# Performance work log

Measured on AMD Instinct MI355X. Metric: run time of the kernel, lower is better.

The kernel has to match this reference:

```python
import jax, jax.numpy as jnp
import numpy as np
from jax import lax

B, T, I, H, L, C = 256, 512, 128, 256, 2, 10


def _lstm_layer(x_tm, lengths, W_ih, W_hh, b_ih, b_hh):
    # x_tm: [T, B, in]; lengths: [B]
    b = b_ih + b_hh  # [4H]
    h0 = jnp.zeros((x_tm.shape[1], H), x_tm.dtype)
    c0 = jnp.zeros_like(h0)

    def step(carry, inp):
        h, c = carry
        x_t, t = inp
        gates = x_t @ W_ih.T + h @ W_hh.T + b  # [B, 4H]
        i, f, g, o = jnp.split(gates, 4, axis=-1)
        i = jax.nn.sigmoid(i); f = jax.nn.sigmoid(f)
        g = jnp.tanh(g);        o = jax.nn.sigmoid(o)
        c_new = f * c + i * g
        h_new = o * jnp.tanh(c_new)
        m = (t < lengths)[:, None]  # freeze state past each sequence's length
        h = jnp.where(m, h_new, h)
        c = jnp.where(m, c_new, c)
        return (h, c), h

    (hT, cT), h_seq = lax.scan(step, (h0, c0), (x_tm, jnp.arange(x_tm.shape[0])))
    return h_seq, hT


def setup_inputs() -> dict:
    key = jax.random.key(0)
    ks = jax.random.split(key, 16)
    s_i = 1.0 / np.sqrt(H)
    inp = {
        'x': jax.random.normal(ks[0], (B, T, I), jnp.float32),
        'lengths': jax.random.randint(ks[1], (B,), 1, T + 1),
        'W_fc': jax.random.uniform(ks[2], (C, H), jnp.float32, -s_i, s_i),
        'b_fc': jax.random.uniform(ks[3], (C,), jnp.float32, -s_i, s_i),
    }
    for l in range(L):
        in_dim = I if l == 0 else H
        k0, k1, k2, k3 = jax.random.split(jax.random.fold_in(key, 100 + l), 4)
        inp[f'W_ih_{l}'] = jax.random.uniform(k0, (4 * H, in_dim), jnp.float32, -s_i, s_i)
        inp[f'W_hh_{l}'] = jax.random.uniform(k1, (4 * H, H), jnp.float32, -s_i, s_i)
        inp[f'b_ih_{l}'] = jax.random.uniform(k2, (4 * H,), jnp.float32, -s_i, s_i)
        inp[f'b_hh_{l}'] = jax.random.uniform(k3, (4 * H,), jnp.float32, -s_i, s_i)
    return inp


def reference(x, lengths, W_fc, b_fc,
              W_ih_0, W_hh_0, b_ih_0, b_hh_0,
              W_ih_1, W_hh_1, b_ih_1, b_hh_1):
    layer_params = [(W_ih_0, W_hh_0, b_ih_0, b_hh_0),
                    (W_ih_1, W_hh_1, b_ih_1, b_hh_1)]
    seq = jnp.swapaxes(x, 0, 1)  # [T, B, I] time-major
    hT = None
    for (W_ih, W_hh, b_ih, b_hh) in layer_params:
        seq, hT = _lstm_layer(seq, lengths, W_ih, W_hh, b_ih, b_hh)
    logits = hT @ W_fc.T + b_fc  # final hidden state of last layer
    return jax.nn.softmax(logits, axis=1)
```

## Files before the change

### kernel.cpp

```cpp
#include <hip/hip_runtime.h>

#define TT 512
#define BB 256
#define II 128
#define HH 256
#define CC 10

typedef __attribute__((ext_vector_type(8))) _Float16 f16x8;
typedef __attribute__((ext_vector_type(4))) _Float16 f16x4;
typedef __attribute__((ext_vector_type(4))) float    f32x4;

__device__ __forceinline__ float fsig(float x){ return 1.0f/(1.0f+__expf(-x)); }
__device__ __forceinline__ float ftanh(float x){ return 2.0f/(1.0f+__expf(-2.0f*x)) - 1.0f; }

__device__ __forceinline__ unsigned cpoll(unsigned* p){
  return __hip_atomic_fetch_add(p, 0u, __ATOMIC_RELAXED, __HIP_MEMORY_SCOPE_AGENT);
}
__device__ __forceinline__ unsigned poll_until(unsigned* p, unsigned tgt){
  unsigned v = 0;
  if((threadIdx.x & 63) == 0){
    v = cpoll(p);
    while(v < tgt){ __builtin_amdgcn_s_sleep(2); v = cpoll(p); }
  }
  unsigned u = __builtin_amdgcn_readfirstlane(v);
  asm volatile("" ::: "memory");
  return u;
}
__device__ __forceinline__ void store_h16(_Float16* p, _Float16 v){
  unsigned b32 = (unsigned)__builtin_bit_cast(unsigned short, v);
  asm volatile("global_store_short %0, %1, off sc0 sc1" :: "v"(p), "v"(b32) : "memory");
}
__device__ __forceinline__ f16x8 load_sc(const _Float16* p){
  f16x8 r;
  asm volatile("global_load_dwordx4 %0, %1, off sc0 sc1" : "=v"(r) : "v"(p) : "memory");
  return r;
}
#define PIN(x) asm volatile("" : "+v"(x))

template<int KXT, bool IS_L1>
__device__ __forceinline__ void run_wave(
    const _Float16* __restrict__ xin,
    const _Float16* __restrict__ Wh,
    const _Float16* __restrict__ Wx,
    const float* __restrict__ b_ih, const float* __restrict__ b_hh,
    const int* __restrict__ lengths,
    _Float16* __restrict__ hbuf,
    float* __restrict__ hT,
    unsigned* cown, unsigned* cprod, int gb, int gj)
{
  constexpr int KXV = KXT*32;
  const int lane = threadIdx.x & 63;
  const int quad = lane >> 4;
  const int l15  = lane & 15;
  const int koff = quad << 3;
  const int b0   = gb << 4;
  const int u    = (gj << 4) + l15;

  f16x8 wh[4][8], wx[4][KXT];
  float bias[4];
#pragma unroll
  for(int g=0; g<4; ++g){
    const int row = g*HH + u;
#pragma unroll
    for(int kt=0; kt<8; ++kt){
      wh[g][kt] = *(const f16x8*)(Wh + (size_t)row*HH + kt*32 + koff);
      PIN(wh[g][kt]);
    }
#pragma unroll
    for(int kt=0; kt<KXT; ++kt){
      wx[g][kt] = *(const f16x8*)(Wx + (size_t)row*KXV + kt*32 + koff);
      PIN(wx[g][kt]);
    }
    bias[g] = b_ih[row] + b_hh[row];
  }

  int sb[4], len[4]; float cs[4], hs[4];
#pragma unroll
  for(int r=0; r<4; ++r){
    sb[r]  = b0 + (quad<<2) + r;
    len[r] = lengths[sb[r]];
    cs[r] = 0.f; hs[r] = 0.f;
  }

  unsigned lastp = 0, lasto = 0;

  f16x8 axn[KXT];
  if(!IS_L1){
    const _Float16* xp = xin + ((size_t)(b0+l15)*TT + 0)*KXV + koff;
#pragma unroll
    for(int kt=0; kt<KXT; ++kt) axn[kt] = *(const f16x8*)(xp + kt*32);
  }

  for(int t=0; t<TT; ++t){
    f16x8 ax[KXT];
    if(IS_L1){
      const unsigned tgtp = 16u*(unsigned)(t+1);
      if(lastp < tgtp) lastp = poll_until(cprod, tgtp);
      const _Float16* xp = xin + ((size_t)t*BB + b0 + l15)*HH + koff;
#pragma unroll
      for(int kt=0; kt<KXT; ++kt) ax[kt] = *(const f16x8*)(xp + kt*32);
    } else {
#pragma unroll
      for(int kt=0; kt<KXT; ++kt) ax[kt] = axn[kt];
    }

    if(t > 0){
      const unsigned tgto = 16u*(unsigned)t;
      if(lasto < tgto) lasto = poll_until(cown, tgto);
    }
    f16x8 ah[8];
    if(t > 0){
      if(IS_L1){
        const _Float16* hp = hbuf + (((size_t)((t-1)&3))*BB + b0 + l15)*HH + koff;
#pragma unroll
        for(int kt=0; kt<8; ++kt) ah[kt] = load_sc(hp + kt*32);
      } else {
        const _Float16* hp = hbuf + ((size_t)(t-1)*BB + b0 + l15)*HH + koff;
#pragma unroll
        for(int kt=0; kt<8; ++kt) ah[kt] = *(const f16x8*)(hp + kt*32);
      }
    }

    f32x4 acc[4];
#pragma unroll
    for(int g=0; g<4; ++g) acc[g] = (f32x4){bias[g],bias[g],bias[g],bias[g]};
#pragma unroll
    for(int kt=0; kt<KXT; ++kt)
#pragma unroll
      for(int g=0; g<4; ++g)
        acc[g] = __builtin_amdgcn_mfma_f32_16x16x32_f16(ax[kt], wx[g][kt], acc[g], 0,0,0);

    if(t > 0){
      if(IS_L1){
        asm volatile("s_waitcnt vmcnt(0)"
          : "+v"(ah[0]),"+v"(ah[1]),"+v"(ah[2]),"+v"(ah[3]),
            "+v"(ah[4]),"+v"(ah[5]),"+v"(ah[6]),"+v"(ah[7]) :: "memory");
      }
#pragma unroll
      for(int kt=0; kt<8; ++kt)
#pragma unroll
        for(int g=0; g<4; ++g)
          acc[g] = __builtin_amdgcn_mfma_f32_16x16x32_f16(ah[kt], wh[g][kt], acc[g], 0,0,0);
    }

#pragma unroll
    for(int r=0; r<4; ++r){
      float iv = fsig (acc[0][r]);
      float fv = fsig (acc[1][r]);
      float gv = ftanh(acc[2][r]);
      float ov = fsig (acc[3][r]);
      float cn = fv*cs[r] + iv*gv;
      float hn = ov*ftanh(cn);
      if(t < len[r]){ cs[r] = cn; hs[r] = hn; }
      _Float16* hp = IS_L1
        ? hbuf + (((size_t)(t&3))*BB + sb[r])*HH + u
        : hbuf + ((size_t)t*BB + sb[r])*HH + u;
      store_h16(hp, (_Float16)hs[r]);
      if(IS_L1 && t == TT-1) hT[(size_t)sb[r]*HH + u] = hs[r];
    }

    asm volatile("s_waitcnt vmcnt(0)" ::: "memory");
    if(lane == 0)
      __hip_atomic_fetch_add(cown, 1u, __ATOMIC_RELAXED, __HIP_MEMORY_SCOPE_AGENT);

    if(!IS_L1 && t+1 < TT){
      const _Float16* xp = xin + ((size_t)(b0+l15)*TT + (t+1))*KXV + koff;
#pragma unroll
      for(int kt=0; kt<KXT; ++kt) axn[kt] = *(const f16x8*)(xp + kt*32);
    }
  }
}

__global__ __launch_bounds__(64, 1)
void lstm_fused(const _Float16* __restrict__ xc,
                const _Float16* __restrict__ Wh0, const _Float16* __restrict__ Wx0,
                const _Float16* __restrict__ Wh1, const _Float16* __restrict__ Wx1,
                const float* __restrict__ b_ih0, const float* __restrict__ b_hh0,
                const float* __restrict__ b_ih1, const float* __restrict__ b_hh1,
                const int* __restrict__ lens,
                _Float16* __restrict__ h0seq, _Float16* __restrict__ h1ring,
                float* __restrict__ hT, unsigned* __restrict__ ctr)
{
  const int blk   = blockIdx.x;
  const int layer = blk >> 8;
  const int gb    = blk & 15;
  const int gj    = (blk >> 4) & 15;
  unsigned* c0 = ctr + gb*32;
  unsigned* c1 = ctr + (16+gb)*32;
  if(layer == 0){
    run_wave<4,false>(xc, Wh0, Wx0, b_ih0, b_hh0, lens, h0seq, nullptr,
                      c0, nullptr, gb, gj);
  } else {
    run_wave<8,true >(h0seq, Wh1, Wx1, b_ih1, b_hh1, lens, h1ring, hT,
                      c1, c0, gb, gj);
  }
}

__global__ __launch_bounds__(256)
void cvt4(const float* __restrict__ in, _Float16* __restrict__ out, int n4)
{
  int i = blockIdx.x*256 + threadIdx.x;
  if(i < n4){
    float4 v = ((const float4*)in)[i];
    f16x4 o;
    o[0]=(_Float16)v.x; o[1]=(_Float16)v.y; o[2]=(_Float16)v.z; o[3]=(_Float16)v.w;
    ((f16x4*)out)[i] = o;
  }
}

__global__ __launch_bounds__(64)
void fc_softmax(const float* __restrict__ hT,
                const float* __restrict__ W_fc,
                const float* __restrict__ b_fc,
                float* __restrict__ out)
{
  const int b = blockIdx.x;
  const int lane = threadIdx.x;
  float p[CC];
#pragma unroll
  for (int c = 0; c < CC; ++c) p[c] = 0.f;
  const float* hb = hT + b * HH;
  for (int k = lane; k < HH; k += 64){
    float hv = hb[k];
#pragma unroll
    for (int c = 0; c < CC; ++c) p[c] += hv * W_fc[c * HH + k];
  }
#pragma unroll
  for (int c = 0; c < CC; ++c){
#pragma unroll
    for (int off = 32; off > 0; off >>= 1) p[c] += __shfl_down(p[c], off);
  }
  if (lane == 0){
    float m = -1e30f;
#pragma unroll
    for (int c = 0; c < CC; ++c){ p[c] += b_fc[c]; m = fmaxf(m, p[c]); }
    float ssum = 0.f;
#pragma unroll
    for (int c = 0; c < CC; ++c){ p[c] = __expf(p[c] - m); ssum += p[c]; }
    float inv = 1.0f / ssum;
#pragma unroll
    for (int c = 0; c < CC; ++c) out[b * CC + c] = p[c] * inv;
  }
}

extern "C" void kernel_launch(void* const* d_in, const int* in_sizes, int n_in,
                              void* d_out, int out_size, void* d_ws, size_t ws_size,
                              hipStream_t stream) {
  const float* x      = (const float*)d_in[0];
  const int*   lens   = (const int*)  d_in[1];
  const float* W_fc   = (const float*)d_in[2];
  const float* b_fc   = (const float*)d_in[3];
  const float* W_ih0  = (const float*)d_in[4];
  const float* W_hh0  = (const float*)d_in[5];
  const float* b_ih0  = (const float*)d_in[6];
  const float* b_hh0  = (const float*)d_in[7];
  const float* W_ih1  = (const float*)d_in[8];
  const float* W_hh1  = (const float*)d_in[9];
  const float* b_ih1  = (const float*)d_in[10];
  const float* b_hh1  = (const float*)d_in[11];
  float* out = (float*)d_out;

  char* ws = (char*)d_ws;
  unsigned* ctr  = (unsigned*)ws;
  float*    hT   = (float*)(ws + 8192);
  _Float16* Wh0c = (_Float16*)(ws + 270336);
  _Float16* Wx0c = (_Float16*)(ws + 794624);
  _Float16* Wh1c = (_Float16*)(ws + 1056768);
  _Float16* Wx1c = (_Float16*)(ws + 1581056);
  _Float16* xc   = (_Float16*)(ws + 2105344);
  _Float16* h0   = (_Float16*)(ws + 35659776);
  _Float16* h1r  = (_Float16*)(ws + 102768640);

  hipMemsetAsync(ws, 0, 8192, stream);

  cvt4<<<dim3((BB*TT*II/4 + 255)/256), dim3(256), 0, stream>>>(x,     xc,   BB*TT*II/4);
  cvt4<<<dim3((4*HH*HH/4  + 255)/256), dim3(256), 0, stream>>>(W_hh0, Wh0c, 4*HH*HH/4);
  cvt4<<<dim3((4*HH*II/4  + 255)/256), dim3(256), 0, stream>>>(W_ih0, Wx0c, 4*HH*II/4);
  cvt4<<<dim3((4*HH*HH/4  + 255)/256), dim3(256), 0, stream>>>(W_hh1, Wh1c, 4*HH*HH/4);
  cvt4<<<dim3((4*HH*HH/4  + 255)/256), dim3(256), 0, stream>>>(W_ih1, Wx1c, 4*HH*HH/4);

  lstm_fused<<<dim3(512), dim3(64), 0, stream>>>(
      xc, Wh0c, Wx0c, Wh1c, Wx1c, b_ih0, b_hh0, b_ih1, b_hh1, lens,
      h0, h1r, hT, ctr);

  fc_softmax<<<dim3(BB), dim3(64), 0, stream>>>(hT, W_fc, b_fc, out);
}
```

Before: 1.802 ms.

## Interleave two batch groups per wave to hide recurrent sync latency

Each wave now handles two independent batch tiles (set and set+8) and alternates between them, so it can signal and poll one tile's counters and issue its h/x loads while computing the other tile's MFMAs and elementwise gates. The grid is halved from 512 to 256 single-wave blocks, each holding the same weight registers but twice the recurrent state. The aim is to cover the cross-block barrier and global-load latency on the serial timestep chain. The cost is double the MFMA work per wave, which lengthens each wave's critical path per step, and half the CUs are left active.

```diff
diff --git a/kernel.cpp b/kernel.cpp
--- a/kernel.cpp
+++ b/kernel.cpp
@@ -13,32 +13,47 @@
 __device__ __forceinline__ float fsig(float x){ return 1.0f/(1.0f+__expf(-x)); }
 __device__ __forceinline__ float ftanh(float x){ return 2.0f/(1.0f+__expf(-2.0f*x)) - 1.0f; }
 
-__device__ __forceinline__ unsigned cpoll(unsigned* p){
-  return __hip_atomic_fetch_add(p, 0u, __ATOMIC_RELAXED, __HIP_MEMORY_SCOPE_AGENT);
-}
-__device__ __forceinline__ unsigned poll_until(unsigned* p, unsigned tgt){
+__device__ __forceinline__ unsigned poll_rmw(unsigned* p, unsigned tgt){
   unsigned v = 0;
   if((threadIdx.x & 63) == 0){
-    v = cpoll(p);
-    while(v < tgt){ __builtin_amdgcn_s_sleep(2); v = cpoll(p); }
+    v = __hip_atomic_fetch_add(p, 0u, __ATOMIC_RELAXED, __HIP_MEMORY_SCOPE_AGENT);
+    while(v < tgt){ __builtin_amdgcn_s_sleep(2);
+      v = __hip_atomic_fetch_add(p, 0u, __ATOMIC_RELAXED, __HIP_MEMORY_SCOPE_AGENT); }
   }
   unsigned u = __builtin_amdgcn_readfirstlane(v);
   asm volatile("" ::: "memory");
   return u;
 }
+__device__ __forceinline__ void arrive(unsigned* p){
+  if((threadIdx.x & 63) == 0)
+    (void)__hip_atomic_fetch_add(p, 1u, __ATOMIC_RELAXED, __HIP_MEMORY_SCOPE_AGENT);
+}
+__device__ __forceinline__ void ld16_sc(f16x8& d, const _Float16* p){
+  asm volatile("global_load_dwordx4 %0, %1, off sc0 sc1" : "=v"(d) : "v"(p) : "memory");
+}
 __device__ __forceinline__ void store_h16(_Float16* p, _Float16 v){
   unsigned b32 = (unsigned)__builtin_bit_cast(unsigned short, v);
   asm volatile("global_store_short %0, %1, off sc0 sc1" :: "v"(p), "v"(b32) : "memory");
 }
-__device__ __forceinline__ f16x8 load_sc(const _Float16* p){
-  f16x8 r;
-  asm volatile("global_load_dwordx4 %0, %1, off sc0 sc1" : "=v"(r) : "v"(p) : "memory");
-  return r;
-}
 #define PIN(x) asm volatile("" : "+v"(x))
 
+__device__ __forceinline__ void ew_store(int t, f32x4 acc[4], float* cs, float* hs,
+    const int* len, _Float16* hbase, int sb0, int u){
+#pragma unroll
+  for(int r=0; r<4; ++r){
+    float iv = fsig (acc[0][r]);
+    float fv = fsig (acc[1][r]);
+    float gv = ftanh(acc[2][r]);
+    float ov = fsig (acc[3][r]);
+    float cn_ = fv*cs[r] + iv*gv;
+    float hn  = ov*ftanh(cn_);
+    if(t < len[r]){ cs[r] = cn_; hs[r] = hn; }
+    store_h16(hbase + (size_t)(sb0+r)*HH + u, (_Float16)hs[r]);
+  }
+}
+
 template<int KXT, bool IS_L1>
-__device__ __forceinline__ void run_wave(
+__device__ __forceinline__ void run_wave2(
     const _Float16* __restrict__ xin,
     const _Float16* __restrict__ Wh,
     const _Float16* __restrict__ Wx,
@@ -46,14 +61,15 @@
     const int* __restrict__ lengths,
     _Float16* __restrict__ hbuf,
     float* __restrict__ hT,
-    unsigned* cown, unsigned* cprod, int gb, int gj)
+    unsigned* __restrict__ ctrL,
+    unsigned* __restrict__ ctrP,
+    int set, int gj)
 {
   constexpr int KXV = KXT*32;
   const int lane = threadIdx.x & 63;
   const int quad = lane >> 4;
   const int l15  = lane & 15;
   const int koff = quad << 3;
-  const int b0   = gb << 4;
   const int u    = (gj << 4) + l15;
 
   f16x8 wh[4][8], wx[4][KXT];
@@ -74,101 +90,131 @@
     bias[g] = b_ih[row] + b_hh[row];
   }
 
-  int sb[4], len[4]; float cs[4], hs[4];
-#pragma unroll
-  for(int r=0; r<4; ++r){
-    sb[r]  = b0 + (quad<<2) + r;
-    len[r] = lengths[sb[r]];
-    cs[r] = 0.f; hs[r] = 0.f;
-  }
-
-  unsigned lastp = 0, lasto = 0;
-
-  f16x8 axn[KXT];
-  if(!IS_L1){
-    const _Float16* xp = xin + ((size_t)(b0+l15)*TT + 0)*KXV + koff;
-#pragma unroll
-    for(int kt=0; kt<KXT; ++kt) axn[kt] = *(const f16x8*)(xp + kt*32);
-  }
-
-  for(int t=0; t<TT; ++t){
-    f16x8 ax[KXT];
-    if(IS_L1){
-      const unsigned tgtp = 16u*(unsigned)(t+1);
-      if(lastp < tgtp) lastp = poll_until(cprod, tgtp);
-      const _Float16* xp = xin + ((size_t)t*BB + b0 + l15)*HH + koff;
-#pragma unroll
-      for(int kt=0; kt<KXT; ++kt) ax[kt] = *(const f16x8*)(xp + kt*32);
-    } else {
-#pragma unroll
-      for(int kt=0; kt<KXT; ++kt) ax[kt] = axn[kt];
-    }
-
-    if(t > 0){
-      const unsigned tgto = 16u*(unsigned)t;
-      if(lasto < tgto) lasto = poll_until(cown, tgto);
-    }
-    f16x8 ah[8];
-    if(t > 0){
-      if(IS_L1){
-        const _Float16* hp = hbuf + (((size_t)((t-1)&3))*BB + b0 + l15)*HH + koff;
-#pragma unroll
-        for(int kt=0; kt<8; ++kt) ah[kt] = load_sc(hp + kt*32);
-      } else {
-        const _Float16* hp = hbuf + ((size_t)(t-1)*BB + b0 + l15)*HH + koff;
-#pragma unroll
-        for(int kt=0; kt<8; ++kt) ah[kt] = *(const f16x8*)(hp + kt*32);
+  const int gb[2] = {set, set + 8};
+  int len[2][4]; float cs[2][4], hs[2][4];
+#pragma unroll
+  for(int c=0; c<2; ++c){
+    const int sb0 = gb[c]*16 + quad*4;
+#pragma unroll
+    for(int r=0; r<4; ++r){
+      len[c][r] = lengths[sb0 + r];
+      cs[c][r] = 0.f; hs[c][r] = 0.f;
+    }
+  }
+  unsigned* cO[2]; unsigned* cQ[2];
+#pragma unroll
+  for(int c=0; c<2; ++c){
+    cO[c] = ctrL + gb[c]*32;
+    cQ[c] = IS_L1 ? (ctrP + gb[c]*32) : nullptr;
+  }
+  unsigned lasto[2] = {0,0}, lastp[2] = {0,0};
+
+  f16x8 ahb[2][8];
+  f16x8 axb[2][KXT];
+
+#pragma unroll
+  for(int c=0; c<2; ++c){
+    if constexpr(IS_L1) lastp[c] = poll_rmw(cQ[c], 16u);
+    f16x8 ax0[KXT];
+    const _Float16* xp = IS_L1
+      ? xin + ((size_t)0*BB + gb[c]*16 + l15)*HH + koff
+      : xin + ((size_t)(gb[c]*16 + l15)*TT + 0)*KXV + koff;
+#pragma unroll
+    for(int kt=0; kt<KXT; ++kt) ax0[kt] = *(const f16x8*)(xp + kt*32);
+    f32x4 acc[4];
+#pragma unroll
+    for(int g=0; g<4; ++g) acc[g] = (f32x4){bias[g],bias[g],bias[g],bias[g]};
+#pragma unroll
+    for(int kt=0; kt<KXT; ++kt)
+#pragma unroll
+      for(int g=0; g<4; ++g)
+        acc[g] = __builtin_amdgcn_mfma_f32_16x16x32_f16(ax0[kt], wx[g][kt], acc[g], 0,0,0);
+    ew_store(0, acc, cs[c], hs[c], len[c], hbuf , gb[c]*16 + quad*4, u);
+    asm volatile("s_waitcnt vmcnt(0)" ::: "memory");
+    if(c == 0) arrive(cO[0]);
+  }
+
+  lasto[0] = poll_rmw(cO[0], 16u);
+  if constexpr(IS_L1){ if(lastp[0] < 32u) lastp[0] = poll_rmw(cQ[0], 32u); }
+  {
+    const _Float16* hp = IS_L1
+      ? hbuf + (((size_t)0)*BB + gb[0]*16 + l15)*HH + koff
+      : hbuf + ((size_t)0*BB + gb[0]*16 + l15)*HH + koff;
+#pragma unroll
+    for(int kt=0; kt<8; ++kt){
+      if constexpr(IS_L1) ld16_sc(ahb[0][kt], hp + kt*32);
+      else                ahb[0][kt] = *(const f16x8*)(hp + kt*32);
+    }
+    const _Float16* xp = IS_L1
+      ? xin + ((size_t)1*BB + gb[0]*16 + l15)*HH + koff
+      : xin + ((size_t)(gb[0]*16 + l15)*TT + 1)*KXV + koff;
+#pragma unroll
+    for(int kt=0; kt<KXT; ++kt) axb[0][kt] = *(const f16x8*)(xp + kt*32);
+  }
+  __builtin_amdgcn_sched_barrier(0);
+
+#pragma unroll 1
+  for(int t=1; t<TT; ++t){
+#pragma unroll
+    for(int c=0; c<2; ++c){
+      const bool fin = (t==TT-1) && (c==1);
+      const int  cn  = 1-c;
+      const int  tn  = (c==0) ? t : t+1;
+
+      asm volatile("s_waitcnt vmcnt(0)" ::: "memory");
+      __builtin_amdgcn_sched_barrier(0);
+      arrive(cO[cn]);
+      if(!fin){
+        const unsigned tgt = 16u*(unsigned)tn;
+        if(lasto[cn] < tgt) lasto[cn] = poll_rmw(cO[cn], tgt);
+        if constexpr(IS_L1){
+          const unsigned tp = 16u*(unsigned)(tn+1);
+          if(lastp[cn] < tp) lastp[cn] = poll_rmw(cQ[cn], tp);
+        }
+        const _Float16* hp = IS_L1
+          ? hbuf + (((size_t)((tn-1)&3))*BB + gb[cn]*16 + l15)*HH + koff
+          : hbuf + ((size_t)(tn-1)*BB + gb[cn]*16 + l15)*HH + koff;
+#pragma unroll
+        for(int kt=0; kt<8; ++kt){
+          if constexpr(IS_L1) ld16_sc(ahb[cn][kt], hp + kt*32);
+          else                ahb[cn][kt] = *(const f16x8*)(hp + kt*32);
+        }
+        const _Float16* xp = IS_L1
+          ? xin + ((size_t)tn*BB + gb[cn]*16 + l15)*HH + koff
+          : xin + ((size_t)(gb[cn]*16 + l15)*TT + tn)*KXV + koff;
+#pragma unroll
+        for(int kt=0; kt<KXT; ++kt) axb[cn][kt] = *(const f16x8*)(xp + kt*32);
+        __builtin_amdgcn_sched_barrier(0);
       }
-    }
-
-    f32x4 acc[4];
-#pragma unroll
-    for(int g=0; g<4; ++g) acc[g] = (f32x4){bias[g],bias[g],bias[g],bias[g]};
-#pragma unroll
-    for(int kt=0; kt<KXT; ++kt)
-#pragma unroll
-      for(int g=0; g<4; ++g)
-        acc[g] = __builtin_amdgcn_mfma_f32_16x16x32_f16(ax[kt], wx[g][kt], acc[g], 0,0,0);
-
-    if(t > 0){
-      if(IS_L1){
-        asm volatile("s_waitcnt vmcnt(0)"
-          : "+v"(ah[0]),"+v"(ah[1]),"+v"(ah[2]),"+v"(ah[3]),
-            "+v"(ah[4]),"+v"(ah[5]),"+v"(ah[6]),"+v"(ah[7]) :: "memory");
+
+      f32x4 acc[4];
+#pragma unroll
+      for(int g=0; g<4; ++g) acc[g] = (f32x4){bias[g],bias[g],bias[g],bias[g]};
+#pragma unroll
+      for(int kt=0; kt<KXT; ++kt)
+#pragma unroll
+        for(int g=0; g<4; ++g)
+          acc[g] = __builtin_amdgcn_mfma_f32_16x16x32_f16(axb[c][kt], wx[g][kt], acc[g], 0,0,0);
+#pragma unroll
+      for(int kt=0; kt<8; ++kt)
+#pragma unroll
+        for(int g=0; g<4; ++g)
+          acc[g] = __builtin_amdgcn_mfma_f32_16x16x32_f16(ahb[c][kt], wh[g][kt], acc[g], 0,0,0);
+
+      _Float16* hbase = IS_L1 ? hbuf + (size_t)(t&3)*BB*HH : hbuf + (size_t)t*BB*HH;
+      const int sb0 = gb[c]*16 + quad*4;
+      ew_store(t, acc, cs[c], hs[c], len[c], hbase, sb0, u);
+      if constexpr(IS_L1){
+        if(t == TT-1){
+#pragma unroll
+          for(int r=0; r<4; ++r) hT[(size_t)(sb0+r)*HH + u] = hs[c][r];
+        }
       }
-#pragma unroll
-      for(int kt=0; kt<8; ++kt)
-#pragma unroll
-        for(int g=0; g<4; ++g)
-          acc[g] = __builtin_amdgcn_mfma_f32_16x16x32_f16(ah[kt], wh[g][kt], acc[g], 0,0,0);
-    }
-
-#pragma unroll
-    for(int r=0; r<4; ++r){
-      float iv = fsig (acc[0][r]);
-      float fv = fsig (acc[1][r]);
-      float gv = ftanh(acc[2][r]);
-      float ov = fsig (acc[3][r]);
-      float cn = fv*cs[r] + iv*gv;
-      float hn = ov*ftanh(cn);
-      if(t < len[r]){ cs[r] = cn; hs[r] = hn; }
-      _Float16* hp = IS_L1
-        ? hbuf + (((size_t)(t&3))*BB + sb[r])*HH + u
-        : hbuf + ((size_t)t*BB + sb[r])*HH + u;
-      store_h16(hp, (_Float16)hs[r]);
-      if(IS_L1 && t == TT-1) hT[(size_t)sb[r]*HH + u] = hs[r];
-    }
-
-    asm volatile("s_waitcnt vmcnt(0)" ::: "memory");
-    if(lane == 0)
-      __hip_atomic_fetch_add(cown, 1u, __ATOMIC_RELAXED, __HIP_MEMORY_SCOPE_AGENT);
-
-    if(!IS_L1 && t+1 < TT){
-      const _Float16* xp = xin + ((size_t)(b0+l15)*TT + (t+1))*KXV + koff;
-#pragma unroll
-      for(int kt=0; kt<KXT; ++kt) axn[kt] = *(const f16x8*)(xp + kt*32);
-    }
-  }
+    }
+  }
+
+  asm volatile("s_waitcnt vmcnt(0)" ::: "memory");
+  arrive(cO[1]);
 }
 
 __global__ __launch_bounds__(64, 1)
@@ -181,18 +227,16 @@
                 _Float16* __restrict__ h0seq, _Float16* __restrict__ h1ring,
                 float* __restrict__ hT, unsigned* __restrict__ ctr)
 {
-  const int blk   = blockIdx.x;
-  const int layer = blk >> 8;
-  const int gb    = blk & 15;
-  const int gj    = (blk >> 4) & 15;
-  unsigned* c0 = ctr + gb*32;
-  unsigned* c1 = ctr + (16+gb)*32;
-  if(layer == 0){
-    run_wave<4,false>(xc, Wh0, Wx0, b_ih0, b_hh0, lens, h0seq, nullptr,
-                      c0, nullptr, gb, gj);
+  const int blk = blockIdx.x;
+  unsigned* c0 = ctr;
+  unsigned* c1 = ctr + 16*32;
+  if(blk < 128){
+    run_wave2<4,false>(xc, Wh0, Wx0, b_ih0, b_hh0, lens, h0seq, nullptr,
+                       c0, nullptr, blk & 7, blk >> 3);
   } else {
-    run_wave<8,true >(h0seq, Wh1, Wx1, b_ih1, b_hh1, lens, h1ring, hT,
-                      c1, c0, gb, gj);
+    const int i = blk - 128;
+    run_wave2<8,true >(h0seq, Wh1, Wx1, b_ih1, b_hh1, lens, h1ring, hT,
+                       c1, c0, i & 7, i >> 3);
   }
 }
 
@@ -279,7 +323,7 @@
   cvt4<<<dim3((4*HH*HH/4  + 255)/256), dim3(256), 0, stream>>>(W_hh1, Wh1c, 4*HH*HH/4);
   cvt4<<<dim3((4*HH*HH/4  + 255)/256), dim3(256), 0, stream>>>(W_ih1, Wx1c, 4*HH*HH/4);
 
-  lstm_fused<<<dim3(512), dim3(64), 0, stream>>>(
+  lstm_fused<<<dim3(256), dim3(64), 0, stream>>>(
       xc, Wh0c, Wx0c, Wh1c, Wx1c, b_ih0, b_hh0, b_ih1, b_hh1, lens,
       h0, h1r, hT, ctr);
 
```

New measurement: 2.968 ms. 64.7% more time.

## Use XCD-local cache scope for inter-block sync when group shares one XCD

Applied to the files above, without the earlier changes.

Each block records its XCC_ID, then all 512 blocks rendezvous on a global counter. A block takes a FAST path only if every block in its batch group (both layers) sits on the same XCD. The FAST path drops the system-scope sc1 bits from h stores, ring loads and counter atomics, which relies on the shared per-XCD L2 for coherence and cuts per-step sync latency. This adds a startup grid barrier, depends on co-residency of all 512 blocks and on the dispatch placement, and probably rarely triggers, since blocks are usually spread round-robin across XCDs.

```diff
diff --git a/kernel.cpp b/kernel.cpp
--- a/kernel.cpp
+++ b/kernel.cpp
@@ -13,31 +13,59 @@
 __device__ __forceinline__ float fsig(float x){ return 1.0f/(1.0f+__expf(-x)); }
 __device__ __forceinline__ float ftanh(float x){ return 2.0f/(1.0f+__expf(-2.0f*x)) - 1.0f; }
 
+
+template<bool FAST>
 __device__ __forceinline__ unsigned cpoll(unsigned* p){
-  return __hip_atomic_fetch_add(p, 0u, __ATOMIC_RELAXED, __HIP_MEMORY_SCOPE_AGENT);
-}
+  unsigned v;
+  if constexpr(FAST){
+    unsigned z = 0u;
+    asm volatile("global_atomic_add %0, %1, %2, off sc0\n\ts_waitcnt vmcnt(0)"
+                 : "=v"(v) : "v"(p), "v"(z) : "memory");
+  } else {
+    v = __hip_atomic_fetch_add(p, 0u, __ATOMIC_RELAXED, __HIP_MEMORY_SCOPE_AGENT);
+  }
+  return v;
+}
+template<bool FAST>
 __device__ __forceinline__ unsigned poll_until(unsigned* p, unsigned tgt){
   unsigned v = 0;
   if((threadIdx.x & 63) == 0){
-    v = cpoll(p);
-    while(v < tgt){ __builtin_amdgcn_s_sleep(2); v = cpoll(p); }
+    v = cpoll<FAST>(p);
+    while(v < tgt){ __builtin_amdgcn_s_sleep(2); v = cpoll<FAST>(p); }
   }
   unsigned u = __builtin_amdgcn_readfirstlane(v);
   asm volatile("" ::: "memory");
   return u;
 }
-__device__ __forceinline__ void store_h16(_Float16* p, _Float16 v){
-  unsigned b32 = (unsigned)__builtin_bit_cast(unsigned short, v);
-  asm volatile("global_store_short %0, %1, off sc0 sc1" :: "v"(p), "v"(b32) : "memory");
-}
-__device__ __forceinline__ f16x8 load_sc(const _Float16* p){
+template<bool FAST>
+__device__ __forceinline__ void arrive1(unsigned* p){
+  if constexpr(FAST){
+    unsigned one = 1u;
+    asm volatile("global_atomic_add %0, %1, off" :: "v"(p), "v"(one) : "memory");
+  } else {
+    (void)__hip_atomic_fetch_add(p, 1u, __ATOMIC_RELAXED, __HIP_MEMORY_SCOPE_AGENT);
+  }
+}
+template<bool FAST>
+__device__ __forceinline__ void store_h16(_Float16* p, _Float16 vv){
+  unsigned b32 = (unsigned)__builtin_bit_cast(unsigned short, vv);
+  if constexpr(FAST)
+    asm volatile("global_store_short %0, %1, off" :: "v"(p), "v"(b32) : "memory");
+  else
+    asm volatile("global_store_short %0, %1, off sc0 sc1" :: "v"(p), "v"(b32) : "memory");
+}
+template<bool FAST>
+__device__ __forceinline__ f16x8 load_ring(const _Float16* p){
   f16x8 r;
-  asm volatile("global_load_dwordx4 %0, %1, off sc0 sc1" : "=v"(r) : "v"(p) : "memory");
+  if constexpr(FAST)
+    asm volatile("global_load_dwordx4 %0, %1, off sc0" : "=v"(r) : "v"(p) : "memory");
+  else
+    asm volatile("global_load_dwordx4 %0, %1, off sc0 sc1" : "=v"(r) : "v"(p) : "memory");
   return r;
 }
 #define PIN(x) asm volatile("" : "+v"(x))
 
-template<int KXT, bool IS_L1>
+template<int KXT, bool IS_L1, bool FAST>
 __device__ __forceinline__ void run_wave(
     const _Float16* __restrict__ xin,
     const _Float16* __restrict__ Wh,
@@ -95,7 +123,7 @@
     f16x8 ax[KXT];
     if(IS_L1){
       const unsigned tgtp = 16u*(unsigned)(t+1);
-      if(lastp < tgtp) lastp = poll_until(cprod, tgtp);
+      if(lastp < tgtp) lastp = poll_until<FAST>(cprod, tgtp);
       const _Float16* xp = xin + ((size_t)t*BB + b0 + l15)*HH + koff;
 #pragma unroll
       for(int kt=0; kt<KXT; ++kt) ax[kt] = *(const f16x8*)(xp + kt*32);
@@ -106,14 +134,14 @@
 
     if(t > 0){
       const unsigned tgto = 16u*(unsigned)t;
-      if(lasto < tgto) lasto = poll_until(cown, tgto);
+      if(lasto < tgto) lasto = poll_until<FAST>(cown, tgto);
     }
     f16x8 ah[8];
     if(t > 0){
       if(IS_L1){
         const _Float16* hp = hbuf + (((size_t)((t-1)&3))*BB + b0 + l15)*HH + koff;
 #pragma unroll
-        for(int kt=0; kt<8; ++kt) ah[kt] = load_sc(hp + kt*32);
+        for(int kt=0; kt<8; ++kt) ah[kt] = load_ring<FAST>(hp + kt*32);
       } else {
         const _Float16* hp = hbuf + ((size_t)(t-1)*BB + b0 + l15)*HH + koff;
 #pragma unroll
@@ -155,13 +183,12 @@
       _Float16* hp = IS_L1
         ? hbuf + (((size_t)(t&3))*BB + sb[r])*HH + u
         : hbuf + ((size_t)t*BB + sb[r])*HH + u;
-      store_h16(hp, (_Float16)hs[r]);
+      store_h16<FAST>(hp, (_Float16)hs[r]);
       if(IS_L1 && t == TT-1) hT[(size_t)sb[r]*HH + u] = hs[r];
     }
 
     asm volatile("s_waitcnt vmcnt(0)" ::: "memory");
-    if(lane == 0)
-      __hip_atomic_fetch_add(cown, 1u, __ATOMIC_RELAXED, __HIP_MEMORY_SCOPE_AGENT);
+    if(lane == 0) arrive1<FAST>(cown);
 
     if(!IS_L1 && t+1 < TT){
       const _Float16* xp = xin + ((size_t)(b0+l15)*TT + (t+1))*KXV + koff;
@@ -185,14 +212,46 @@
   const int layer = blk >> 8;
   const int gb    = blk & 15;
   const int gj    = (blk >> 4) & 15;
-  unsigned* c0 = ctr + gb*32;
-  unsigned* c1 = ctr + (16+gb)*32;
+  const int lane  = threadIdx.x & 63;
+  unsigned* c0    = ctr + gb*32;
+  unsigned* c1    = ctr + (16+gb)*32;
+  unsigned* xcds  = ctr + 1024;
+  unsigned* cinit = ctr + 1536;
+
+  unsigned myx;
+  asm volatile("s_getreg_b32 %0, hwreg(HW_REG_XCC_ID)" : "=s"(myx));
+  if(lane == 0){
+    asm volatile("global_store_dword %0, %1, off sc0 sc1" :: "v"(xcds + blk), "v"(myx) : "memory");
+    asm volatile("s_waitcnt vmcnt(0)" ::: "memory");
+    (void)__hip_atomic_fetch_add(cinit, 1u, __ATOMIC_RELAXED, __HIP_MEMORY_SCOPE_AGENT);
+  }
+  unsigned iv = 0;
+  if(lane == 0){
+    iv = __hip_atomic_fetch_add(cinit, 0u, __ATOMIC_RELAXED, __HIP_MEMORY_SCOPE_AGENT);
+    while(iv < 512u){ __builtin_amdgcn_s_sleep(8);
+      iv = __hip_atomic_fetch_add(cinit, 0u, __ATOMIC_RELAXED, __HIP_MEMORY_SCOPE_AGENT); }
+  }
+  (void)__builtin_amdgcn_readfirstlane(iv);
+  asm volatile("" ::: "memory");
+  unsigned pv = myx;
+  if(lane < 32){
+    const unsigned* pp = xcds + ((lane < 16) ? (gb + 16*lane)
+                                             : (256 + gb + 16*(lane-16)));
+    asm volatile("global_load_dword %0, %1, off sc0 sc1\n\ts_waitcnt vmcnt(0)"
+                 : "=v"(pv) : "v"(pp) : "memory");
+  }
+  const bool fast = (__ballot(pv == myx) == ~0ull);
+
   if(layer == 0){
-    run_wave<4,false>(xc, Wh0, Wx0, b_ih0, b_hh0, lens, h0seq, nullptr,
-                      c0, nullptr, gb, gj);
+    if(fast) run_wave<4,false,true >(xc, Wh0, Wx0, b_ih0, b_hh0, lens, h0seq,
+                                     nullptr, c0, nullptr, gb, gj);
+    else     run_wave<4,false,false>(xc, Wh0, Wx0, b_ih0, b_hh0, lens, h0seq,
+                                     nullptr, c0, nullptr, gb, gj);
   } else {
-    run_wave<8,true >(h0seq, Wh1, Wx1, b_ih1, b_hh1, lens, h1ring, hT,
-                      c1, c0, gb, gj);
+    if(fast) run_wave<8,true ,true >(h0seq, Wh1, Wx1, b_ih1, b_hh1, lens, h1ring,
+                                     hT, c1, c0, gb, gj);
+    else     run_wave<8,true ,false>(h0seq, Wh1, Wx1, b_ih1, b_hh1, lens, h1ring,
+                                     hT, c1, c0, gb, gj);
   }
 }
 
```

Measured after the change: 1.476 ms. 1.22x faster.
